# Optimization experiments

Measured on AMD Instinct MI355X. Metric: run time of the kernel, lower is better.

The kernel has to match this reference:

```python
import jax, jax.numpy as jnp
import numpy as np

COMMIT_WEIGHT = 0.25


def setup_inputs() -> dict:
    key = jax.random.key(0)
    k1, k2 = jax.random.split(key)
    B, D, T, K = 8, 512, 2048, 8192
    x = jax.random.normal(k1, (B, D, T), dtype=jnp.float32)
    codebook = jax.random.normal(k2, (K, D), dtype=jnp.float32)
    return {"x": x, "codebook": codebook}


def reference(x, codebook):
    # x: [B, D, T] channels-first; VQ operates on [B, T, D]
    xt = jnp.transpose(x, (0, 2, 1))  # [B, T, D]
    x2 = jnp.sum(xt * xt, axis=-1, keepdims=True)          # [B, T, 1]
    e2 = jnp.sum(codebook * codebook, axis=-1)             # [K]
    xe = jnp.einsum('btd,kd->btk', xt, codebook)           # [B, T, K] (dominant GEMM)
    dists = x2 - 2.0 * xe + e2                             # [B, T, K]
    indices = jnp.argmin(dists, axis=-1)                   # [B, T] int
    quantized = codebook[indices]                          # [B, T, D] gather
    # commitment loss: ||sg(q) - x||^2 mean
    commit_loss = COMMIT_WEIGHT * jnp.mean(
        (jax.lax.stop_gradient(quantized) - xt) ** 2)
    # straight-through estimator
    quantized = xt + jax.lax.stop_gradient(quantized - xt)
    quantized = jnp.transpose(quantized, (0, 2, 1))        # back to [B, D, T]
    return quantized, indices, commit_loss
```

## Files before the change

### kernel.cpp

```cpp
#include <hip/hip_runtime.h>
#include <cstdint>
#include <cstddef>

#define B_   8
#define D_   512
#define T_   2048
#define K_   8192
#define BT_  (B_ * T_)
#define NQ_  ((size_t)B_ * D_ * T_)

typedef _Float16 f16x8 __attribute__((ext_vector_type(8)));
typedef _Float16 f16x4 __attribute__((ext_vector_type(4)));
typedef float    f32x4 __attribute__((ext_vector_type(4)));
typedef unsigned long long u64;
typedef unsigned int u32;

#define WS_SLOTS_OFF    0
#define WS_FIDX_OFF     393216
#define WS_PART_OFF     458752
#define WS_E2_OFF       460800
#define WS_XH_OFF       524288
#define WS_XL_OFF       (WS_XH_OFF + 16777216)
#define WS_CH_OFF       (WS_XL_OFF + 16777216)
#define WS_NEEDED       ((size_t)WS_CH_OFF + 8388608)

__device__ __forceinline__ void gload_lds16(const void* g, void* l) {
    __builtin_amdgcn_global_load_lds(
        (const __attribute__((address_space(1))) void*)g,
        (__attribute__((address_space(3))) void*)l, 16, 0, 0);
}

__device__ __forceinline__ u32 fkey(float f) {
    u32 u = __float_as_uint(f);
    u ^= (u32)((int)u >> 31) | 0x80000000u;
    return u;
}
__device__ __forceinline__ u64 umin64(u64 a, u64 b) { return a < b ? a : b; }
__device__ __forceinline__ u64 umax64(u64 a, u64 b) { return a > b ? a : b; }

__global__ __launch_bounds__(256) void k_e2(const float* __restrict__ cb,
                                            float* __restrict__ e2) {
    int k = blockIdx.x * 256 + threadIdx.x;
    const float4* row = (const float4*)(cb + (size_t)k * D_);
    float s = 0.f;
#pragma unroll 4
    for (int i = 0; i < D_ / 4; ++i) {
        float4 v = row[i];
        s = fmaf(v.x, v.x, s); s = fmaf(v.y, v.y, s);
        s = fmaf(v.z, v.z, s); s = fmaf(v.w, v.w, s);
    }
    e2[k] = s;
}

__global__ __launch_bounds__(256) void k_splitcb(const float* __restrict__ cb,
                                                 _Float16* __restrict__ ch) {
    size_t i = ((size_t)blockIdx.x * 256 + threadIdx.x) * 4;
    float4 v = *(const float4*)(cb + i);
    f16x4 h;
    h[0] = (_Float16)v.x; h[1] = (_Float16)v.y;
    h[2] = (_Float16)v.z; h[3] = (_Float16)v.w;
    *(f16x4*)(ch + i) = h;
}

__global__ __launch_bounds__(256) void k_splitx(const float* __restrict__ x,
                                                _Float16* __restrict__ xh,
                                                _Float16* __restrict__ xl) {
    int b  = blockIdx.z;
    int d0 = blockIdx.y * 64;
    int t0 = blockIdx.x * 64;
    int dl = threadIdx.x & 63;
    int tq = threadIdx.x >> 6;
    const float* px = x + ((size_t)b * D_ + (d0 + dl)) * T_ + t0;
#pragma unroll 4
    for (int i = 0; i < 16; ++i) {
        int t = tq * 16 + i;
        float v = px[t];
        _Float16 h = (_Float16)v;
        float lo = v - (float)h;
        _Float16 l = (_Float16)lo;
        size_t row = (size_t)b * T_ + t0 + t;
        xh[row * D_ + d0 + dl] = h;
        xl[row * D_ + d0 + dl] = l;
    }
}

__global__ __launch_bounds__(512, 2)
void k_hi_argmin(const _Float16* __restrict__ xh, const _Float16* __restrict__ ch,
                 const float* __restrict__ e2, u64* __restrict__ slots) {
    __shared__ char smem[131072];
    __shared__ u32 stop[256][2][2];
    __shared__ float e2s[1024];

    const int tid = threadIdx.x;
    const int xcd = blockIdx.x & 7;
    const int bi  = blockIdx.x >> 3;
    const int m_  = bi >> 3;
    const int nblk = bi & 7;
    const int mbase  = (xcd * 8 + m_) * 256;
    const int nstart = nblk * 1024;

    const int lane = tid & 63;
    const int wid  = tid >> 6;
    const int wr = wid & 3, wc = wid >> 2;
    const int lr = lane & 15, lg = lane >> 4;

    {
        u32* p = (u32*)stop;
        p[tid] = ~0u; p[tid + 512] = ~0u;
        *(float2*)&e2s[tid * 2] = *(const float2*)&e2[nstart + tid * 2];
    }
    __syncthreads();

    const bool isA = wid < 4;
    const int q8 = lane >> 3;
    const int u8 = (lane & 7) ^ q8;
    const int srow2 = (u8 >> 2) & 1;
    const int sslot = u8 & 3;
    const char* gs0 = isA
        ? (const char*)xh + (size_t)(mbase  + (wid & 3) * 64 + 2 * q8 + srow2) * 1024
              + sslot * 16
        : (const char*)ch + (size_t)(nstart + (wid & 3) * 64 + 2 * q8 + srow2) * 1024
              + sslot * 16;
    const int ldsbase = (isA ? 0 : 16384) + (wid & 3) * 4096;

#define STAGE2(g, i0) do {                                                   \
        char* lb_ = smem + ((g) & 3) * 32768 + ldsbase;                      \
        const char* gs_ = gs0 + (isA ? 0 : (size_t)((g) >> 4) * 262144)      \
                          + ((g) & 15) * 64;                                 \
        gload_lds16(gs_ + (size_t)(i0) * 16384, lb_ + (i0) * 1024);          \
        gload_lds16(gs_ + (size_t)((i0) + 1) * 16384, lb_ + ((i0) + 1) * 1024); \
    } while (0)

    const int lrh = lr >> 1;
    const int swz16 = ((lg + 4 * (lr & 1)) ^ lrh) * 16;
    const int aoff0 = (wr * 32 + lrh) * 128 + swz16;
    const int boff0 = 16384 + (wc * 64 + lrh) * 128 + swz16;

    u32 top2a[16], top2b[16];
#pragma unroll
    for (int s = 0; s < 16; ++s) { top2a[s] = ~0u; top2b[s] = ~0u; }

    f32x4 acc[4][8];
#pragma unroll
    for (int m = 0; m < 4; ++m)
#pragma unroll
        for (int n = 0; n < 8; ++n)
            acc[m][n] = (f32x4){0.f, 0.f, 0.f, 0.f};

    auto epilogue = [&](int ns) {
        float e2v[8];
#pragma unroll
        for (int n = 0; n < 8; ++n)
            e2v[n] = 0.5f * e2s[ns * 256 + wc * 128 + n * 16 + lr];
        const u32 base10 = ((u32)ns << 8) | ((u32)wc << 7) | (u32)lr;
#pragma unroll
        for (int m = 0; m < 4; ++m) {
#pragma unroll
            for (int j = 0; j < 4; ++j) {
                const int s = m * 4 + j;
                u32 t1 = top2a[s], t2 = top2b[s];
#pragma unroll
                for (int n = 0; n < 8; ++n) {
                    float d = fmaxf(e2v[n] - acc[m][n][j], 1.0f);
                    u32 p = (__float_as_uint(d) & 0xFFFFFC00u) | (base10 + ((u32)n << 4));
                    u32 mx = t1 > p ? t1 : p;
                    t1 = t1 < p ? t1 : p;
                    t2 = t2 < mx ? t2 : mx;
                }
                top2a[s] = t1; top2b[s] = t2;
            }
        }
#pragma unroll
        for (int m = 0; m < 4; ++m)
#pragma unroll
            for (int n = 0; n < 8; ++n)
                acc[m][n] = (f32x4){0.f, 0.f, 0.f, 0.f};
    };

#define MFMA16(AF, BF, NOFF)                                                 \
        _Pragma("unroll")                                                    \
        for (int m = 0; m < 4; ++m)                                          \
            _Pragma("unroll")                                                \
            for (int n = 0; n < 4; ++n)                                      \
                acc[m][(NOFF) + n] = __builtin_amdgcn_mfma_f32_16x16x32_f16( \
                    AF[m], BF[n], acc[m][(NOFF) + n], 0, 0, 0);

    STAGE2(0, 0); STAGE2(0, 2);
    STAGE2(1, 0); STAGE2(1, 2);
    asm volatile("s_waitcnt vmcnt(0)" ::: "memory");
    __builtin_amdgcn_s_barrier();

#pragma unroll 1
    for (int p = 0; p < 32; ++p) {
        const char* baseA = smem + ((2 * p) & 3) * 32768;
        const char* baseB = smem + ((2 * p + 1) & 3) * 32768;

        if (p < 31) {
            STAGE2(2 * p + 2, 0); STAGE2(2 * p + 2, 2);
            STAGE2(2 * p + 3, 0); STAGE2(2 * p + 3, 2);
        }

        f16x8 af0[4], af1[4], bf[4], bg[4];
#pragma unroll
        for (int m = 0; m < 4; ++m)
            af0[m] = *(const f16x8*)(baseA + aoff0 + m * 1024);
#pragma unroll
        for (int n = 0; n < 4; ++n)
            bf[n] = *(const f16x8*)(baseA + boff0 + n * 1024);
#pragma unroll
        for (int n = 0; n < 4; ++n)
            bg[n] = *(const f16x8*)(baseA + boff0 + (4 + n) * 1024);
#pragma unroll
        for (int m = 0; m < 4; ++m)
            af1[m] = *(const f16x8*)(baseB + aoff0 + m * 1024);

        MFMA16(af0, bf, 0)

#pragma unroll
        for (int n = 0; n < 4; ++n)
            bf[n] = *(const f16x8*)(baseB + boff0 + n * 1024);

        MFMA16(af0, bg, 4)

#pragma unroll
        for (int n = 0; n < 4; ++n)
            bg[n] = *(const f16x8*)(baseB + boff0 + (4 + n) * 1024);

        MFMA16(af1, bf, 0)
        MFMA16(af1, bg, 4)

        asm volatile("s_waitcnt lgkmcnt(0)" ::: "memory");
        asm volatile("s_waitcnt vmcnt(0)" ::: "memory");
        __builtin_amdgcn_s_barrier();
        if ((p & 7) == 7) epilogue(p >> 3);
    }
#undef STAGE2
#undef MFMA16

#pragma unroll
    for (int m = 0; m < 4; ++m) {
#pragma unroll
        for (int j = 0; j < 4; ++j) {
            const int s = m * 4 + j;
            u32 t1 = top2a[s], t2 = top2b[s];
#pragma unroll
            for (int st = 1; st < 16; st <<= 1) {
                u32 o1 = __shfl_xor(t1, st);
                u32 o2 = __shfl_xor(t2, st);
                u32 mx = t1 > o1 ? t1 : o1;
                u32 sel = t1 < o1 ? t2 : o2;
                u32 n2 = mx < sel ? mx : sel;
                t1 = t1 < o1 ? t1 : o1;
                t2 = t2 < n2 ? t2 : n2;
            }
            if (lr == 0) {
                int ql = wr * 64 + m * 16 + lg * 4 + j;
                stop[ql][wc][0] = t1; stop[ql][wc][1] = t2;
            }
        }
    }

    __syncthreads();
    if (tid < 256) {
        u32 a1 = stop[tid][0][0], a2 = stop[tid][0][1];
        u32 b1 = stop[tid][1][0], b2 = stop[tid][1][1];
        u32 f1 = a1 < b1 ? a1 : b1;
        u32 mx = a1 > b1 ? a1 : b1;
        u32 sel = a1 < b1 ? a2 : b2;
        u32 f2 = mx < sel ? mx : sel;
        int q = mbase + tid;
        u64 p1 = ((u64)(f1 & 0xFFFFFC00u) << 32) | (u32)(nstart + (f1 & 0x3FFu));
        u64 p2 = ((u64)(f2 & 0xFFFFFC00u) << 32) | (u32)(nstart + (f2 & 0x3FFu));
        u64* As = slots + q;
        u64* Bs = slots + BT_ + q;
        u64* Cs = slots + 2 * BT_ + q;
        u64 old = atomicMin(As, p1);
        u64 v = umax64(old, p1);
        old = atomicMin(Bs, v);
        u64 v2 = umax64(old, v);
        atomicMin(Cs, v2);
        old = atomicMin(Bs, p2);
        v = umax64(old, p2);
        atomicMin(Cs, v);
    }
}

__global__ __launch_bounds__(256)
void k_rescore(const _Float16* __restrict__ xh, const _Float16* __restrict__ xl,
               const float* __restrict__ cb, const float* __restrict__ e2,
               const u64* __restrict__ slots,
               u32* __restrict__ final_idx, float* __restrict__ out_idx) {
    const int wid = threadIdx.x >> 6, lane = threadIdx.x & 63;
    const int q = blockIdx.x * 4 + wid;
    u64 a = slots[q], b = slots[BT_ + q], c = slots[2 * BT_ + q];
    u32 i1 = (u32)a, i2 = (u32)b, i3 = (u32)c;
    float d1 = __uint_as_float((u32)(a >> 32));
    float d2 = __uint_as_float((u32)(b >> 32));
    u32 win = i1;
    if (!(d2 - d1 > 0.75f)) {
        float xr[8];
        f16x8 hv = *(const f16x8*)(xh + (size_t)q * D_ + lane * 8);
        f16x8 lv = *(const f16x8*)(xl + (size_t)q * D_ + lane * 8);
#pragma unroll
        for (int i = 0; i < 8; ++i) xr[i] = (float)hv[i] + (float)lv[i];
        u32 idxs[3] = {i1, i2, i3};
        float key[3];
#pragma unroll 1
        for (int cnd = 0; cnd < 3; ++cnd) {
            const float4* cr = (const float4*)(cb + (size_t)idxs[cnd] * D_ + lane * 8);
            float4 c0 = cr[0], c1 = cr[1];
            float s = xr[0] * c0.x;
            s = fmaf(xr[1], c0.y, s); s = fmaf(xr[2], c0.z, s); s = fmaf(xr[3], c0.w, s);
            s = fmaf(xr[4], c1.x, s); s = fmaf(xr[5], c1.y, s);
            s = fmaf(xr[6], c1.z, s); s = fmaf(xr[7], c1.w, s);
#pragma unroll
            for (int st = 1; st < 64; st <<= 1) s += __shfl_xor(s, st);
            key[cnd] = e2[idxs[cnd]] - 2.f * s;
        }
        float bk = key[0]; win = idxs[0];
#pragma unroll
        for (int cnd = 1; cnd < 3; ++cnd) {
            if (key[cnd] < bk || (key[cnd] == bk && idxs[cnd] < win)) {
                bk = key[cnd]; win = idxs[cnd];
            }
        }
    }
    if (lane == 0) { final_idx[q] = win; out_idx[q] = (float)win; }
}

#define MB 64
#define NB 64
#define KC 32
#define FNSPLIT 2
#define KPER (K_ / FNSPLIT)
__global__ __launch_bounds__(256, 2)
void k_argmin_f32(const float* __restrict__ x, const float* __restrict__ cb,
                  const float* __restrict__ e2, u64* __restrict__ slots) {
    __shared__ float xs[KC][MB + 4];
    __shared__ float es[KC][NB + 4];
    __shared__ u64 red[MB];
    const int tid = threadIdx.x;
    const int tx = tid & 15, ty = tid >> 4;
    const int rowtile = blockIdx.x;
    const int b = rowtile >> 5;
    const int tbase = (rowtile & 31) * MB;
    const int nstart = blockIdx.y * KPER;
    if (tid < MB) red[tid] = ~0ull;
    float bestv[4]; int besti[4];
#pragma unroll
    for (int i = 0; i < 4; ++i) { bestv[i] = 3.4e38f; besti[i] = 0; }
    const int sm = tid & 63, sg = tid >> 6;
    const float* xbase = x + (size_t)b * D_ * T_ + (tbase + sm);
    for (int nb = 0; nb < KPER; nb += NB) {
        float acc[4][4];
#pragma unroll
        for (int i = 0; i < 4; ++i)
#pragma unroll
            for (int j = 0; j < 4; ++j) acc[i][j] = 0.f;
        for (int kc = 0; kc < D_; kc += KC) {
            __syncthreads();
#pragma unroll
            for (int r = 0; r < 8; ++r) {
                int dd = sg * 8 + r;
                xs[dd][sm] = xbase[(size_t)(kc + dd) * T_];
            }
            const float* crow = cb + (size_t)(nstart + nb + sm) * D_ + kc + sg * 8;
            float4 c0 = *(const float4*)(crow);
            float4 c1 = *(const float4*)(crow + 4);
            es[sg * 8 + 0][sm] = c0.x; es[sg * 8 + 1][sm] = c0.y;
            es[sg * 8 + 2][sm] = c0.z; es[sg * 8 + 3][sm] = c0.w;
            es[sg * 8 + 4][sm] = c1.x; es[sg * 8 + 5][sm] = c1.y;
            es[sg * 8 + 6][sm] = c1.z; es[sg * 8 + 7][sm] = c1.w;
            __syncthreads();
#pragma unroll
            for (int dd = 0; dd < KC; ++dd) {
                float4 a = *(const float4*)&xs[dd][tx * 4];
                float4 e = *(const float4*)&es[dd][ty * 4];
                acc[0][0] = fmaf(a.x, e.x, acc[0][0]); acc[0][1] = fmaf(a.x, e.y, acc[0][1]);
                acc[0][2] = fmaf(a.x, e.z, acc[0][2]); acc[0][3] = fmaf(a.x, e.w, acc[0][3]);
                acc[1][0] = fmaf(a.y, e.x, acc[1][0]); acc[1][1] = fmaf(a.y, e.y, acc[1][1]);
                acc[1][2] = fmaf(a.y, e.z, acc[1][2]); acc[1][3] = fmaf(a.y, e.w, acc[1][3]);
                acc[2][0] = fmaf(a.z, e.x, acc[2][0]); acc[2][1] = fmaf(a.z, e.y, acc[2][1]);
                acc[2][2] = fmaf(a.z, e.z, acc[2][2]); acc[2][3] = fmaf(a.z, e.w, acc[2][3]);
                acc[3][0] = fmaf(a.w, e.x, acc[3][0]); acc[3][1] = fmaf(a.w, e.y, acc[3][1]);
                acc[3][2] = fmaf(a.w, e.z, acc[3][2]); acc[3][3] = fmaf(a.w, e.w, acc[3][3]);
            }
        }
#pragma unroll
        for (int j = 0; j < 4; ++j) {
            int c = nstart + nb + ty * 4 + j;
            float ec = e2[c];
#pragma unroll
            for (int i = 0; i < 4; ++i) {
                float dist = fmaf(-2.f, acc[i][j], ec);
                if (dist < bestv[i]) { bestv[i] = dist; besti[i] = c; }
            }
        }
    }
    __syncthreads();
#pragma unroll
    for (int i = 0; i < 4; ++i) {
        u64 p = ((u64)fkey(bestv[i]) << 32) | (u32)besti[i];
        atomicMin(&red[tx * 4 + i], p);
    }
    __syncthreads();
    if (tid < MB) atomicMin(&slots[b * T_ + tbase + tid], red[tid]);
}

__global__ __launch_bounds__(256)
void k_finalize(const u64* __restrict__ slots,
                u32* __restrict__ final_idx, float* __restrict__ out_idx) {
    int q = blockIdx.x * 256 + threadIdx.x;
    u32 idx = (u32)slots[q];
    final_idx[q] = idx;
    out_idx[q] = (float)idx;
}

__global__ __launch_bounds__(256)
void k_gather(const float* __restrict__ x, const float* __restrict__ cb,
              const u32* __restrict__ final_idx,
              float* __restrict__ out_q, float* __restrict__ partials) {
    int tid = threadIdx.x;
    int btg = blockIdx.x * 256 + tid;
    int b = btg >> 11, t = btg & (T_ - 1);
    int dch = blockIdx.y;
    u32 idx = final_idx[btg];
    const float* crow = cb + (size_t)idx * D_;
    size_t xoff = (size_t)b * D_ * T_ + t;
    float ls = 0.f;
#pragma unroll 4
    for (int dd = 0; dd < 64; ++dd) {
        int d = dch * 64 + dd;
        float q = crow[d];
        size_t o = xoff + (size_t)d * T_;
        float xv = x[o];
        out_q[o] = q;
        float df = q - xv;
        ls = fmaf(df, df, ls);
    }
    __shared__ float rs[256];
    rs[tid] = ls;
    __syncthreads();
    for (int s = 128; s > 0; s >>= 1) {
        if (tid < s) rs[tid] += rs[tid + s];
        __syncthreads();
    }
    if (tid == 0) partials[blockIdx.y * 64 + blockIdx.x] = rs[0];
}

__global__ __launch_bounds__(256)
void k_loss(const float* __restrict__ partials, float* __restrict__ out_loss) {
    __shared__ float rs[256];
    int tid = threadIdx.x;
    float s = partials[tid] + partials[tid + 256];
    rs[tid] = s;
    __syncthreads();
    for (int st = 128; st > 0; st >>= 1) {
        if (tid < st) rs[tid] += rs[tid + st];
        __syncthreads();
    }
    if (tid == 0) out_loss[0] = 0.25f * rs[0] / (float)NQ_;
}

extern "C" void kernel_launch(void* const* d_in, const int* in_sizes, int n_in,
                              void* d_out, int out_size, void* d_ws, size_t ws_size,
                              hipStream_t stream) {
    const float* x  = (const float*)d_in[0];
    const float* cb = (const float*)d_in[1];

    float* out_q    = (float*)d_out;
    float* out_idx  = out_q + NQ_;
    float* out_loss = out_idx + BT_;

    char* ws = (char*)d_ws;
    u64* slots = (u64*)(ws + WS_SLOTS_OFF);
    u32* fidx = (u32*)(ws + WS_FIDX_OFF);
    float* partials = (float*)(ws + WS_PART_OFF);
    float* e2 = (float*)(ws + WS_E2_OFF);

    hipMemsetAsync(slots, 0xFF, (size_t)3 * BT_ * 8, stream);
    k_e2<<<dim3(K_ / 256), dim3(256), 0, stream>>>(cb, e2);

    if (ws_size >= WS_NEEDED) {
        _Float16* xhp = (_Float16*)(ws + WS_XH_OFF);
        _Float16* xlp = (_Float16*)(ws + WS_XL_OFF);
        _Float16* chp = (_Float16*)(ws + WS_CH_OFF);
        k_splitcb<<<dim3((K_ * D_ / 4) / 256), dim3(256), 0, stream>>>(cb, chp);
        k_splitx<<<dim3(T_ / 64, D_ / 64, B_), dim3(256), 0, stream>>>(x, xhp, xlp);
        k_hi_argmin<<<dim3(512), dim3(512), 0, stream>>>(xhp, chp, e2, slots);
        k_rescore<<<dim3(BT_ / 4), dim3(256), 0, stream>>>(xhp, xlp, cb, e2, slots,
                                                           fidx, out_idx);
    } else {
        k_argmin_f32<<<dim3(BT_ / MB, FNSPLIT), dim3(256), 0, stream>>>(x, cb, e2, slots);
        k_finalize<<<dim3(BT_ / 256), dim3(256), 0, stream>>>(slots, fidx, out_idx);
    }

    k_gather<<<dim3(BT_ / 256, D_ / 64), dim3(256), 0, stream>>>(x, cb, fidx,
                                                                 out_q, partials);
    k_loss<<<dim3(1), dim3(256), 0, stream>>>(partials, out_loss);
}
```

Baseline: 215.1 us.

## Load A fragments directly to registers and halve block tile in argmin GEMM

The high-precision argmin GEMM now uses 256-thread blocks with 128-row M tiles and twice as many blocks. The x operand is read from global memory straight into registers rather than being staged through LDS, so LDS holds only codebook tiles and shrinks to 64KB. It also adds a partial vmcnt wait so the next stage's loads can stay in flight across the barrier, plus s_setprio around the MFMA bursts. The trade-off is less A reuse per block, more global traffic for x, and register loads whose latency may not be fully hidden.

```diff
diff --git a/kernel.cpp b/kernel.cpp
--- a/kernel.cpp
+++ b/kernel.cpp
@@ -84,57 +84,54 @@
     }
 }
 
-__global__ __launch_bounds__(512, 2)
+__global__ __launch_bounds__(256, 2)
 void k_hi_argmin(const _Float16* __restrict__ xh, const _Float16* __restrict__ ch,
                  const float* __restrict__ e2, u64* __restrict__ slots) {
-    __shared__ char smem[131072];
-    __shared__ u32 stop[256][2][2];
-    __shared__ float e2s[1024];
+    __shared__ __align__(16) char smem[65536];
+    __shared__ u32 stop[128][2][2];
+    __shared__ __align__(16) float e2s[1024];
 
     const int tid = threadIdx.x;
     const int xcd = blockIdx.x & 7;
     const int bi  = blockIdx.x >> 3;
     const int m_  = bi >> 3;
     const int nblk = bi & 7;
-    const int mbase  = (xcd * 8 + m_) * 256;
+    const int mbase  = (xcd * 16 + m_) * 128;
     const int nstart = nblk * 1024;
 
     const int lane = tid & 63;
     const int wid  = tid >> 6;
-    const int wr = wid & 3, wc = wid >> 2;
+    const int wr = wid & 1, wc = wid >> 1;
     const int lr = lane & 15, lg = lane >> 4;
 
     {
         u32* p = (u32*)stop;
-        p[tid] = ~0u; p[tid + 512] = ~0u;
-        *(float2*)&e2s[tid * 2] = *(const float2*)&e2[nstart + tid * 2];
+        p[tid] = ~0u; p[tid + 256] = ~0u;
+        *(float4*)&e2s[tid * 4] = *(const float4*)&e2[nstart + tid * 4];
     }
     __syncthreads();
 
-    const bool isA = wid < 4;
     const int q8 = lane >> 3;
     const int u8 = (lane & 7) ^ q8;
     const int srow2 = (u8 >> 2) & 1;
     const int sslot = u8 & 3;
-    const char* gs0 = isA
-        ? (const char*)xh + (size_t)(mbase  + (wid & 3) * 64 + 2 * q8 + srow2) * 1024
-              + sslot * 16
-        : (const char*)ch + (size_t)(nstart + (wid & 3) * 64 + 2 * q8 + srow2) * 1024
-              + sslot * 16;
-    const int ldsbase = (isA ? 0 : 16384) + (wid & 3) * 4096;
-
-#define STAGE2(g, i0) do {                                                   \
-        char* lb_ = smem + ((g) & 3) * 32768 + ldsbase;                      \
-        const char* gs_ = gs0 + (isA ? 0 : (size_t)((g) >> 4) * 262144)      \
-                          + ((g) & 15) * 64;                                 \
-        gload_lds16(gs_ + (size_t)(i0) * 16384, lb_ + (i0) * 1024);          \
-        gload_lds16(gs_ + (size_t)((i0) + 1) * 16384, lb_ + ((i0) + 1) * 1024); \
+    const char* gs0 = (const char*)ch
+        + (size_t)(nstart + wid * 64 + 2 * q8 + srow2) * 1024 + sslot * 16;
+    const int ldsb = wid * 4096;
+
+#define STAGEB(g) do {                                                       \
+        char* lb_ = smem + ((g) & 3) * 16384 + ldsb;                         \
+        const char* gs_ = gs0 + (size_t)((g) >> 4) * 262144 + ((g) & 15) * 64; \
+        _Pragma("unroll")                                                    \
+        for (int i_ = 0; i_ < 4; ++i_)                                       \
+            gload_lds16(gs_ + (size_t)i_ * 16384, lb_ + i_ * 1024);          \
     } while (0)
 
     const int lrh = lr >> 1;
     const int swz16 = ((lg + 4 * (lr & 1)) ^ lrh) * 16;
-    const int aoff0 = (wr * 32 + lrh) * 128 + swz16;
-    const int boff0 = 16384 + (wc * 64 + lrh) * 128 + swz16;
+    const int boff0 = (wc * 64 + lrh) * 128 + swz16;
+
+    const _Float16* arow = xh + (size_t)(mbase + wr * 64 + lr) * 512 + lg * 8;
 
     u32 top2a[16], top2b[16];
 #pragma unroll
@@ -185,56 +182,62 @@
                 acc[m][(NOFF) + n] = __builtin_amdgcn_mfma_f32_16x16x32_f16( \
                     AF[m], BF[n], acc[m][(NOFF) + n], 0, 0, 0);
 
-    STAGE2(0, 0); STAGE2(0, 2);
-    STAGE2(1, 0); STAGE2(1, 2);
+    f16x8 afE[4], afO[4], bf[4], bg[4];
+
+    STAGEB(0); STAGEB(1);
+#pragma unroll
+    for (int m = 0; m < 4; ++m)
+        afE[m] = *(const f16x8*)(arow + m * 8192);
     asm volatile("s_waitcnt vmcnt(0)" ::: "memory");
     __builtin_amdgcn_s_barrier();
 
 #pragma unroll 1
     for (int p = 0; p < 32; ++p) {
-        const char* baseA = smem + ((2 * p) & 3) * 32768;
-        const char* baseB = smem + ((2 * p + 1) & 3) * 32768;
+        const char* baseA_ = smem + ((2 * p) & 3) * 16384;
+        const char* baseB_ = smem + ((2 * p + 1) & 3) * 16384;
+
+        if (p < 31) { STAGEB(2 * p + 2); STAGEB(2 * p + 3); }
+        __builtin_amdgcn_sched_barrier(0);
+
+#pragma unroll
+        for (int m = 0; m < 4; ++m)
+            afO[m] = *(const f16x8*)(arow + m * 8192 + ((2 * p + 1) & 15) * 32);
+
+#pragma unroll
+        for (int n = 0; n < 4; ++n)
+            bf[n] = *(const f16x8*)(baseA_ + boff0 + n * 1024);
+#pragma unroll
+        for (int n = 0; n < 4; ++n)
+            bg[n] = *(const f16x8*)(baseA_ + boff0 + (4 + n) * 1024);
+        __builtin_amdgcn_s_setprio(1);
+        MFMA16(afE, bf, 0)
+        MFMA16(afE, bg, 4)
+        __builtin_amdgcn_s_setprio(0);
 
         if (p < 31) {
-            STAGE2(2 * p + 2, 0); STAGE2(2 * p + 2, 2);
-            STAGE2(2 * p + 3, 0); STAGE2(2 * p + 3, 2);
-        }
-
-        f16x8 af0[4], af1[4], bf[4], bg[4];
-#pragma unroll
-        for (int m = 0; m < 4; ++m)
-            af0[m] = *(const f16x8*)(baseA + aoff0 + m * 1024);
+#pragma unroll
+            for (int m = 0; m < 4; ++m)
+                afE[m] = *(const f16x8*)(arow + m * 8192 + ((2 * p + 2) & 15) * 32);
+        }
+
 #pragma unroll
         for (int n = 0; n < 4; ++n)
-            bf[n] = *(const f16x8*)(baseA + boff0 + n * 1024);
+            bf[n] = *(const f16x8*)(baseB_ + boff0 + n * 1024);
 #pragma unroll
         for (int n = 0; n < 4; ++n)
-            bg[n] = *(const f16x8*)(baseA + boff0 + (4 + n) * 1024);
-#pragma unroll
-        for (int m = 0; m < 4; ++m)
-            af1[m] = *(const f16x8*)(baseB + aoff0 + m * 1024);
-
-        MFMA16(af0, bf, 0)
-
-#pragma unroll
-        for (int n = 0; n < 4; ++n)
-            bf[n] = *(const f16x8*)(baseB + boff0 + n * 1024);
-
-        MFMA16(af0, bg, 4)
-
-#pragma unroll
-        for (int n = 0; n < 4; ++n)
-            bg[n] = *(const f16x8*)(baseB + boff0 + (4 + n) * 1024);
-
-        MFMA16(af1, bf, 0)
-        MFMA16(af1, bg, 4)
+            bg[n] = *(const f16x8*)(baseB_ + boff0 + (4 + n) * 1024);
+        __builtin_amdgcn_s_setprio(1);
+        MFMA16(afO, bf, 0)
+        MFMA16(afO, bg, 4)
+        __builtin_amdgcn_s_setprio(0);
 
         asm volatile("s_waitcnt lgkmcnt(0)" ::: "memory");
-        asm volatile("s_waitcnt vmcnt(0)" ::: "memory");
+        if (p < 31) asm volatile("s_waitcnt vmcnt(4)" ::: "memory");
+        else        asm volatile("s_waitcnt vmcnt(0)" ::: "memory");
         __builtin_amdgcn_s_barrier();
         if ((p & 7) == 7) epilogue(p >> 3);
     }
-#undef STAGE2
+#undef STAGEB
 #undef MFMA16
 
 #pragma unroll
@@ -261,7 +264,7 @@
     }
 
     __syncthreads();
-    if (tid < 256) {
+    if (tid < 128) {
         u32 a1 = stop[tid][0][0], a2 = stop[tid][0][1];
         u32 b1 = stop[tid][1][0], b2 = stop[tid][1][1];
         u32 f1 = a1 < b1 ? a1 : b1;
@@ -487,7 +490,7 @@
         _Float16* chp = (_Float16*)(ws + WS_CH_OFF);
         k_splitcb<<<dim3((K_ * D_ / 4) / 256), dim3(256), 0, stream>>>(cb, chp);
         k_splitx<<<dim3(T_ / 64, D_ / 64, B_), dim3(256), 0, stream>>>(x, xhp, xlp);
-        k_hi_argmin<<<dim3(512), dim3(512), 0, stream>>>(xhp, chp, e2, slots);
+        k_hi_argmin<<<dim3(1024), dim3(256), 0, stream>>>(xhp, chp, e2, slots);
         k_rescore<<<dim3(BT_ / 4), dim3(256), 0, stream>>>(xhp, xlp, cb, e2, slots,
                                                            fidx, out_idx);
     } else {
```

After: 251.2 us. +16.8%, slower.
